# Performance work log

Measured on AMD Instinct MI355X. Metric: run time of the kernel, lower is better.

The kernel has to match this reference:

```python
import jax, jax.numpy as jnp
import numpy as np

D_MODEL = 512; D_STATE = 64; D_CONV = 4; HEADDIM = 64
D_INNER = 2 * D_MODEL              # expand=2
NHEADS = D_INNER // HEADDIM        # 16
CONV_DIM = D_INNER + 2 * D_STATE   # 1152
D_IN_PROJ = 2 * D_INNER + 2 * D_STATE + NHEADS  # 2192
BATCH, SEQ = 4, 1024
EPS = 1e-5


def rmsnorm(x, w):
    return x * jax.lax.rsqrt(jnp.mean(x * x, axis=-1, keepdims=True) + EPS) * w


def mamba2(u, in_w, conv_w, conv_b, dt_bias, A_log, D, gnorm_w, out_w):
    b, l, _ = u.shape
    zxbcdt = u @ in_w.T                                  # [b,l,D_IN_PROJ]
    z = zxbcdt[..., :D_INNER]
    xBC = zxbcdt[..., D_INNER:D_INNER + CONV_DIM]
    dt = jax.nn.softplus(zxbcdt[..., -NHEADS:] + dt_bias)  # [b,l,h]
    # causal depthwise conv1d (kernel D_CONV, left pad) + silu
    pad = jnp.pad(xBC, ((0, 0), (D_CONV - 1, 0), (0, 0)))
    acc = conv_b
    for k in range(D_CONV):
        acc = acc + pad[:, k:k + l, :] * conv_w[:, k]
    xBC = jax.nn.silu(acc)
    x = xBC[..., :D_INNER].reshape(b, l, NHEADS, HEADDIM)
    Bm = xBC[..., D_INNER:D_INNER + D_STATE]             # [b,l,n]
    Cm = xBC[..., D_INNER + D_STATE:]                    # [b,l,n]
    A = -jnp.exp(A_log)                                  # [h]
    decay = jnp.exp(dt * A)                              # [b,l,h]
    dtx = dt[..., None] * x                              # [b,l,h,p]

    def step(h, inp):
        dec, dx, Bt, Ct = inp
        h = h * dec[:, :, None, None] + dx[..., None] * Bt[:, None, None, :]
        y = jnp.einsum('bhpn,bn->bhp', h, Ct)
        return h, y

    h0 = jnp.zeros((b, NHEADS, HEADDIM, D_STATE), u.dtype)
    _, ys = jax.lax.scan(step, h0, (decay.transpose(1, 0, 2),
                                    dtx.transpose(1, 0, 2, 3),
                                    Bm.transpose(1, 0, 2),
                                    Cm.transpose(1, 0, 2)))
    y = ys.transpose(1, 0, 2, 3) + x * D[None, None, :, None]  # [b,l,h,p]
    y = y.reshape(b, l, D_INNER)
    y = rmsnorm(y * jax.nn.silu(z), gnorm_w)             # gated RMSNorm
    return y @ out_w.T


def setup_inputs() -> dict:
    key = jax.random.key(0)
    ks = iter(jax.random.split(key, 32))
    def rn(shape, scale=0.02):
        return jax.random.normal(next(ks), shape, dtype=jnp.float32) * scale
    inp = {
        'x': jax.random.normal(next(ks), (BATCH, SEQ, D_MODEL), dtype=jnp.float32),
        'norm_w': jnp.ones((D_MODEL,), jnp.float32),
    }
    for p in ('f', 'b'):
        inp[p + '_in_w'] = rn((D_IN_PROJ, D_MODEL))
        inp[p + '_conv_w'] = rn((CONV_DIM, D_CONV), 0.1)
        inp[p + '_conv_b'] = jnp.zeros((CONV_DIM,), jnp.float32)
        inp[p + '_dt_bias'] = rn((NHEADS,), 0.5)
        inp[p + '_A_log'] = jnp.log(jnp.arange(1, NHEADS + 1, dtype=jnp.float32))
        inp[p + '_D'] = jnp.ones((NHEADS,), jnp.float32)
        inp[p + '_gnorm_w'] = jnp.ones((D_INNER,), jnp.float32)
        inp[p + '_out_w'] = rn((D_MODEL, D_INNER))
    inp['proj_w'] = rn((D_MODEL, 2 * D_MODEL))
    return inp


def reference(x, norm_w,
              f_in_w, f_conv_w, f_conv_b, f_dt_bias, f_A_log, f_D, f_gnorm_w, f_out_w,
              b_in_w, b_conv_w, b_conv_b, b_dt_bias, b_A_log, b_D, b_gnorm_w, b_out_w,
              proj_w):
    h = rmsnorm(x, norm_w)
    fo = mamba2(h, f_in_w, f_conv_w, f_conv_b, f_dt_bias, f_A_log, f_D, f_gnorm_w, f_out_w)
    bo = jnp.flip(mamba2(jnp.flip(h, 1), b_in_w, b_conv_w, b_conv_b, b_dt_bias,
                         b_A_log, b_D, b_gnorm_w, b_out_w), 1)
    return x + jnp.concatenate([fo, bo], axis=-1) @ proj_w.T
```

## Files before the change

### kernel.cpp

```cpp
#include <hip/hip_runtime.h>
#include <math.h>

typedef unsigned short u16;
typedef __bf16  bf16x8 __attribute__((ext_vector_type(8)));
typedef float   f32x4  __attribute__((ext_vector_type(4)));
typedef unsigned short u16x8 __attribute__((ext_vector_type(8)));

#define SEQ 1024
#define MR  4096
#define DIP 2192
#define DI  1024
#define NH  16
#define CD  1152
#define NCH 32
#define CT  32
#define NIN (DIP*512)
#define NOUT (512*1024)
#define ZROW 4384

__device__ __forceinline__ u16 f2bf(float f) {
  union { float f; unsigned u; } v; v.f = f;
  unsigned r = v.u + 0x7FFFu + ((v.u >> 16) & 1u);
  return (u16)(r >> 16);
}
__device__ __forceinline__ float bf2f(u16 h) {
  union { unsigned u; float f; } v; v.u = ((unsigned)h) << 16; return v.f;
}
__device__ __forceinline__ void splitbf(float v, u16& h, u16& l) {
  h = f2bf(v); l = f2bf(v - bf2f(h));
}
__device__ __forceinline__ float sigm(float x){ return 1.f/(1.f+__expf(-x)); }

__device__ __forceinline__ unsigned packbf(float v) {
  u16 hh, ll; splitbf(v, hh, ll);
  return (unsigned)hh | ((unsigned)ll << 16);
}
__device__ __forceinline__ float unpackf(unsigned w) {
  return bf2f((u16)w) + bf2f((u16)(w >> 16));
}

__device__ __forceinline__ void unpack8(const unsigned* p, bf16x8& H, bf16x8& L) {
  uint4 a = *(const uint4*)p, b = *(const uint4*)(p+4);
  u16x8 hu, lu;
  hu[0]=(u16)a.x; lu[0]=(u16)(a.x>>16);
  hu[1]=(u16)a.y; lu[1]=(u16)(a.y>>16);
  hu[2]=(u16)a.z; lu[2]=(u16)(a.z>>16);
  hu[3]=(u16)a.w; lu[3]=(u16)(a.w>>16);
  hu[4]=(u16)b.x; lu[4]=(u16)(b.x>>16);
  hu[5]=(u16)b.y; lu[5]=(u16)(b.y>>16);
  hu[6]=(u16)b.z; lu[6]=(u16)(b.z>>16);
  hu[7]=(u16)b.w; lu[7]=(u16)(b.w>>16);
  H = __builtin_bit_cast(bf16x8, hu);
  L = __builtin_bit_cast(bf16x8, lu);
}
__device__ __forceinline__ void unpack8s(const unsigned* p, int stride, bf16x8& H, bf16x8& L) {
  u16x8 hu, lu;
  #pragma unroll
  for (int jj=0;jj<8;jj++){ unsigned w = p[(size_t)jj*stride]; hu[jj]=(u16)w; lu[jj]=(u16)(w>>16); }
  H = __builtin_bit_cast(bf16x8, hu);
  L = __builtin_bit_cast(bf16x8, lu);
}

__device__ __forceinline__ void gl16(const u16* g, u16* l) {
  __builtin_amdgcn_global_load_lds((const __attribute__((address_space(1))) void*)g,
                                   (__attribute__((address_space(3))) void*)l,
                                   16, 0, 0);
}

__global__ __launch_bounds__(256) void cast_all(
  const float* __restrict__ f_in, const float* __restrict__ b_in,
  const float* __restrict__ f_out, const float* __restrict__ b_out,
  const float* __restrict__ proj,
  u16* __restrict__ H, u16* __restrict__ L)
{
  int i = blockIdx.x*256 + threadIdx.x;
  constexpr int TOT = 2*NIN + 3*NOUT;
  if (i >= TOT) return;
  float v;
  if (i < NIN)               v = f_in[i];
  else if (i < 2*NIN)        v = b_in[i-NIN];
  else if (i < 2*NIN+NOUT)   v = f_out[i-2*NIN];
  else if (i < 2*NIN+2*NOUT) v = b_out[i-2*NIN-NOUT];
  else                       v = proj[i-2*NIN-2*NOUT];
  u16 hh, ll; splitbf(v, hh, ll);
  H[i] = hh; L[i] = ll;
}

__global__ __launch_bounds__(256) void rmsnorm_x(const float* __restrict__ x,
                                                 const float* __restrict__ w,
                                                 u16* __restrict__ hbh,
                                                 u16* __restrict__ hbl){
  int m = blockIdx.x, tid = threadIdx.x;
  const float* xr = x + (size_t)m*512;
  float2 v = *(const float2*)&xr[tid*2];
  float ss = v.x*v.x + v.y*v.y;
  #pragma unroll
  for (int off=32; off; off>>=1) ss += __shfl_xor(ss, off, 64);
  __shared__ float red[4];
  if ((tid&63)==0) red[tid>>6] = ss;
  __syncthreads();
  float total = red[0]+red[1]+red[2]+red[3];
  float rs = rsqrtf(total*(1.f/512.f) + 1e-5f);
  float2 w2 = *(const float2*)&w[tid*2];
  u16 h0,l0,h1,l1;
  splitbf(v.x*rs*w2.x, h0, l0);
  splitbf(v.y*rs*w2.y, h1, l1);
  *(unsigned*)&hbh[(size_t)m*512 + tid*2] = (unsigned)h0 | ((unsigned)h1<<16);
  *(unsigned*)&hbl[(size_t)m*512 + tid*2] = (unsigned)l0 | ((unsigned)l1<<16);
}

__global__ __launch_bounds__(256) void gemm_in(
    const u16* __restrict__ Ah, const u16* __restrict__ Al,
    const u16* __restrict__ Wh, const u16* __restrict__ Wl,
    float* __restrict__ C0)
{
  constexpr int K = 512;
  constexpr int N = DIP;
  __shared__ __align__(16) u16 sAh[128*32];
  __shared__ __align__(16) u16 sAl[128*32];
  __shared__ __align__(16) u16 sBh[128*32];
  __shared__ __align__(16) u16 sBl[128*32];
  const int tid = threadIdx.x;
  const int dir = blockIdx.z;
  const int m0 = blockIdx.x * 128;
  const int n0 = blockIdx.y * 128;
  const int lane = tid & 63;
  const int wid  = tid >> 6;
  const u16* wh_p = Wh + (size_t)dir*NIN;
  const u16* wl_p = Wl + (size_t)dir*NIN;
  const int j0 = wid, j1 = wid + 4;
  const int cp = lane & 3;
  auto goff = [&](int j, bool isB)->size_t {
    int row = 16*j + (lane>>2);
    int s = (row>>1) & 3;
    int kc = (cp ^ s) * 8;
    int grow;
    if (!isB) {
      grow = m0 + row;
      if (dir) grow = (grow & ~1023) + (1023 - (grow & 1023));
    } else {
      grow = n0 + row;
      if (grow >= N) grow = N-1;
    }
    return (size_t)grow*K + kc;
  };
  const size_t a0 = goff(j0,false), a1 = goff(j1,false);
  const size_t b0 = goff(j0,true),  b1 = goff(j1,true);
  const int wm = (wid & 1) * 64;
  const int wn = (wid >> 1) * 64;
  const int quad = lane >> 4;
  const int l16  = lane & 15;
  const int qx = quad ^ ((l16>>1)&3);
  const int baseA = ((wm + l16)*4 + qx)*8;
  const int baseB = ((wn + l16)*4 + qx)*8;
  f32x4 acc[4][4] = {};
  for (int kt = 0; kt < K; kt += 32) {
    __syncthreads();
    gl16(Ah + a0 + kt, &sAh[j0*512]);  gl16(Ah + a1 + kt, &sAh[j1*512]);
    gl16(Al + a0 + kt, &sAl[j0*512]);  gl16(Al + a1 + kt, &sAl[j1*512]);
    gl16(wh_p + b0 + kt, &sBh[j0*512]);  gl16(wh_p + b1 + kt, &sBh[j1*512]);
    gl16(wl_p + b0 + kt, &sBl[j0*512]);  gl16(wl_p + b1 + kt, &sBl[j1*512]);
    __syncthreads();
    bf16x8 ah[4], al[4], bh[4], bl[4];
    #pragma unroll
    for (int i=0;i<4;i++) {
      ah[i] = *(const bf16x8*)&sAh[baseA + i*512];
      al[i] = *(const bf16x8*)&sAl[baseA + i*512];
    }
    #pragma unroll
    for (int j=0;j<4;j++) {
      bh[j] = *(const bf16x8*)&sBh[baseB + j*512];
      bl[j] = *(const bf16x8*)&sBl[baseB + j*512];
    }
    #pragma unroll
    for (int i=0;i<4;i++)
      #pragma unroll
      for (int j=0;j<4;j++) {
        f32x4 t = __builtin_amdgcn_mfma_f32_16x16x32_bf16(ah[i], bl[j], acc[i][j], 0,0,0);
        t       = __builtin_amdgcn_mfma_f32_16x16x32_bf16(al[i], bh[j], t,         0,0,0);
        acc[i][j] = __builtin_amdgcn_mfma_f32_16x16x32_bf16(ah[i], bh[j], t,       0,0,0);
      }
  }
  #pragma unroll
  for (int i=0;i<4;i++)
  #pragma unroll
  for (int j=0;j<4;j++)
  #pragma unroll
  for (int r=0;r<4;r++) {
    int mo = m0 + wm + i*16 + quad*4 + r;
    int no = n0 + wn + j*16 + l16;
    if (no < N) C0[((size_t)dir*MR + mo)*DIP + no] = acc[i][j][r];
  }
}

template<int MODE>
__global__ __launch_bounds__(256) void gemm_out(
    const u16* __restrict__ Ah, const u16* __restrict__ Al,
    const u16* __restrict__ Wh, const u16* __restrict__ Wl,
    float* __restrict__ C0, const float* __restrict__ X0,
    u16* __restrict__ C1h, u16* __restrict__ C1l)
{
  constexpr int K = 1024;
  constexpr int AS = (MODE==1) ? ZROW : 1024;
  __shared__ __align__(16) u16 sAh[64*32];
  __shared__ __align__(16) u16 sAl[64*32];
  __shared__ __align__(16) u16 sBh[128*32];
  __shared__ __align__(16) u16 sBl[128*32];
  const int tid = threadIdx.x;
  const int dir = blockIdx.z;
  const int m0 = blockIdx.x * 64;
  const int n0 = blockIdx.y * 128;
  const int lane = tid & 63;
  const int wid  = tid >> 6;
  const u16* ah_p = Ah + ((MODE==1) ? (size_t)dir*MR*AS : 0);
  const u16* al_p = Al + ((MODE==1) ? (size_t)dir*MR*AS : 0);
  const u16* wh_p = Wh + ((MODE==1) ? (size_t)dir*NOUT : 0);
  const u16* wl_p = Wl + ((MODE==1) ? (size_t)dir*NOUT : 0);
  const int cp = lane & 3;
  auto goff = [&](int j, bool isB)->size_t {
    int row = 16*j + (lane>>2);
    int s = (row>>1) & 3;
    int kc = (cp ^ s) * 8;
    int grow = (isB ? n0 : m0) + row;
    return (size_t)grow*(isB ? (size_t)K : (size_t)AS) + kc;
  };
  const size_t a0 = goff(wid,false);
  const size_t b0 = goff(wid,true), b1 = goff(wid+4,true);
  const int quad = lane >> 4;
  const int l16  = lane & 15;
  const int qx = quad ^ ((l16>>1)&3);
  const int baseA = (l16*4 + qx)*8;
  const int baseB = ((wid*32 + l16)*4 + qx)*8;
  f32x4 acc[4][2] = {};
  for (int kt = 0; kt < K; kt += 32) {
    __syncthreads();
    gl16(ah_p + a0 + kt, &sAh[wid*512]);
    gl16(al_p + a0 + kt, &sAl[wid*512]);
    gl16(wh_p + b0 + kt, &sBh[wid*512]);  gl16(wh_p + b1 + kt, &sBh[(wid+4)*512]);
    gl16(wl_p + b0 + kt, &sBl[wid*512]);  gl16(wl_p + b1 + kt, &sBl[(wid+4)*512]);
    __syncthreads();
    bf16x8 ah[4], al[4], bh[2], bl[2];
    #pragma unroll
    for (int i=0;i<4;i++) {
      ah[i] = *(const bf16x8*)&sAh[baseA + i*512];
      al[i] = *(const bf16x8*)&sAl[baseA + i*512];
    }
    #pragma unroll
    for (int j=0;j<2;j++) {
      bh[j] = *(const bf16x8*)&sBh[baseB + j*512];
      bl[j] = *(const bf16x8*)&sBl[baseB + j*512];
    }
    #pragma unroll
    for (int i=0;i<4;i++)
      #pragma unroll
      for (int j=0;j<2;j++) {
        f32x4 t = __builtin_amdgcn_mfma_f32_16x16x32_bf16(ah[i], bl[j], acc[i][j], 0,0,0);
        t       = __builtin_amdgcn_mfma_f32_16x16x32_bf16(al[i], bh[j], t,         0,0,0);
        acc[i][j] = __builtin_amdgcn_mfma_f32_16x16x32_bf16(ah[i], bh[j], t,       0,0,0);
      }
  }
  #pragma unroll
  for (int i=0;i<4;i++)
  #pragma unroll
  for (int j=0;j<2;j++)
  #pragma unroll
  for (int r=0;r<4;r++) {
    int mo = m0 + i*16 + quad*4 + r;
    int no = n0 + wid*32 + j*16 + l16;
    float v = acc[i][j][r];
    if (MODE==1) {
      int ro = mo;
      if (dir) ro = (mo & ~1023) + (1023 - (mo & 1023));
      u16 hh, ll; splitbf(v, hh, ll);
      C1h[(size_t)ro*DI + dir*512 + no] = hh;
      C1l[(size_t)ro*DI + dir*512 + no] = ll;
    } else {
      C0[(size_t)mo*512 + no] = v + X0[(size_t)mo*512 + no];
    }
  }
}

__global__ __launch_bounds__(320) void conv_dt(
  const float* __restrict__ Z,
  const float* __restrict__ f_cw, const float* __restrict__ f_cb,
  const float* __restrict__ b_cw, const float* __restrict__ b_cb,
  const float* __restrict__ f_dtb, const float* __restrict__ b_dtb,
  unsigned* __restrict__ xconv,
  unsigned* __restrict__ Bc, unsigned* __restrict__ Cc,
  float* __restrict__ dtq)
{
  int bm = blockIdx.x;
  int dir = bm >> 12;
  int t = bm & 1023;
  const float* cw  = dir ? b_cw : f_cw;
  const float* cb  = dir ? b_cb : f_cb;
  const float* dtb = dir ? b_dtb : f_dtb;
  int tid = threadIdx.x;
  if (tid < 288) {
    int c0 = tid*4;
    const float* zbase = Z + (size_t)(bm-3)*DIP + 1024 + c0;
    float4 w0 = *(const float4*)&cw[c0*4];
    float4 w1 = *(const float4*)&cw[(c0+1)*4];
    float4 w2 = *(const float4*)&cw[(c0+2)*4];
    float4 w3 = *(const float4*)&cw[(c0+3)*4];
    float4 z0 = {0,0,0,0}, z1 = {0,0,0,0}, z2 = {0,0,0,0};
    float4 z3 = *(const float4*)(zbase + 3*(size_t)DIP);
    if (t >= 3) {
      z0 = *(const float4*)(zbase);
      z1 = *(const float4*)(zbase + (size_t)DIP);
      z2 = *(const float4*)(zbase + 2*(size_t)DIP);
    } else {
      if (t >= 1) z2 = *(const float4*)(zbase + 2*(size_t)DIP);
      if (t >= 2) z1 = *(const float4*)(zbase + (size_t)DIP);
    }
    float4 a = *(const float4*)&cb[c0];
    a.x += z0.x*w0.x + z1.x*w0.y + z2.x*w0.z + z3.x*w0.w;
    a.y += z0.y*w1.x + z1.y*w1.y + z2.y*w1.z + z3.y*w1.w;
    a.z += z0.z*w2.x + z1.z*w2.y + z2.z*w2.z + z3.z*w2.w;
    a.w += z0.w*w3.x + z1.w*w3.y + z2.w*w3.z + z3.w*w3.w;
    float4 v;
    v.x = a.x * sigm(a.x); v.y = a.y * sigm(a.y);
    v.z = a.z * sigm(a.z); v.w = a.w * sigm(a.w);
    uint4 pv;
    pv.x = packbf(v.x); pv.y = packbf(v.y);
    pv.z = packbf(v.z); pv.w = packbf(v.w);
    if (c0 < 1024)      *(uint4*)&xconv[(size_t)bm*DI + c0] = pv;
    else if (c0 < 1088) *(uint4*)&Bc[(size_t)bm*64 + (c0-1024)] = pv;
    else                *(uint4*)&Cc[(size_t)bm*64 + (c0-1088)] = pv;
  }
  if (tid < NH) {
    float dtraw = Z[(size_t)bm*DIP + 2176 + tid] + dtb[tid];
    float dt = (dtraw > 20.f) ? dtraw : log1pf(__expf(dtraw));
    dtq[(size_t)bm*NH + tid] = dt;
  }
}

__global__ __launch_bounds__(256) void scan_mfma(
  const float* __restrict__ dtq, const unsigned* __restrict__ xconv,
  const unsigned* __restrict__ Bc, const unsigned* __restrict__ Cc,
  const float* __restrict__ f_Al, const float* __restrict__ b_Al,
  float* __restrict__ yraw, float* __restrict__ cumdec, float* __restrict__ S)
{
  __shared__ __align__(16) u16 sMh[4][32*40];
  __shared__ __align__(16) u16 sMl[4][32*40];
  __shared__ float scum[4][32];
  __shared__ float sdt[4][32];
  int bx = blockIdx.x;
  int hq = bx & 3, chunk = (bx>>2)&(NCH-1), dirb = bx>>7;
  int w = threadIdx.x >> 6, lane = threadIdx.x & 63;
  int h = hq*4 + w;
  int base_row = dirb*1024 + chunk*CT;
  const int quad = lane >> 4, l16 = lane & 15;
  const float* Al = (dirb >= 4) ? b_Al : f_Al;
  float A = -__expf(Al[h]);
  float dtl = 0.f, cum = 0.f;
  if (lane < 32) { dtl = dtq[(size_t)(base_row + lane)*16 + h]; cum = dtl; }
  #pragma unroll
  for (int off=1; off<32; off<<=1) {
    int src = (lane >= off) ? lane-off : lane;
    float o = __shfl(cum, src);
    if (lane >= off && lane < 32) cum += o;
  }
  if (lane < 32) {
    sdt[w][lane]  = dtl;
    scum[w][lane] = cum;
    cumdec[(size_t)(base_row + lane)*16 + h] = __expf(A*cum);
  }
  bf16x8 chf[2][2], clf[2][2], bhf[2][2], blf[2][2];
  #pragma unroll
  for (int i=0;i<2;i++)
  #pragma unroll
  for (int kk=0;kk<2;kk++) {
    unpack8(Cc + (size_t)(base_row + 16*i + l16)*64 + kk*32 + quad*8, chf[i][kk], clf[i][kk]);
    unpack8(Bc + (size_t)(base_row + 16*i + l16)*64 + kk*32 + quad*8, bhf[i][kk], blf[i][kk]);
  }
  f32x4 g[2][2];
  __builtin_amdgcn_s_setprio(1);
  #pragma unroll
  for (int i=0;i<2;i++)
  #pragma unroll
  for (int j=0;j<2;j++) {
    f32x4 acc = {};
    #pragma unroll
    for (int kk=0;kk<2;kk++) {
      acc = __builtin_amdgcn_mfma_f32_16x16x32_bf16(chf[i][kk], blf[j][kk], acc, 0,0,0);
      acc = __builtin_amdgcn_mfma_f32_16x16x32_bf16(clf[i][kk], bhf[j][kk], acc, 0,0,0);
      acc = __builtin_amdgcn_mfma_f32_16x16x32_bf16(chf[i][kk], bhf[j][kk], acc, 0,0,0);
    }
    g[i][j] = acc;
  }
  __builtin_amdgcn_s_setprio(0);
  float ctt[2][4];
  #pragma unroll
  for (int i=0;i<2;i++)
  #pragma unroll
  for (int r=0;r<4;r++) ctt[i][r] = scum[w][16*i + quad*4 + r];
  #pragma unroll
  for (int j=0;j<2;j++) {
    int s = 16*j + l16;
    float cts = scum[w][s];
    float dts = sdt[w][s];
    #pragma unroll
    for (int i=0;i<2;i++)
    #pragma unroll
    for (int r=0;r<4;r++) {
      int t = 16*i + quad*4 + r;
      float mv = (s <= t) ? g[i][j][r] * __expf(A*(ctt[i][r]-cts)) * dts : 0.f;
      u16 hh, ll; splitbf(mv, hh, ll);
      sMh[w][t*40 + s] = hh;
      sMl[w][t*40 + s] = ll;
    }
  }
  bf16x8 xhf[4], xlf[4];
  const unsigned* xp = xconv + (size_t)(base_row + quad*8)*1024 + h*64 + l16;
  #pragma unroll
  for (int jp=0;jp<4;jp++) unpack8s(xp + 16*jp, 1024, xhf[jp], xlf[jp]);
  bf16x8 mhf[2], mlf[2];
  #pragma unroll
  for (int i=0;i<2;i++) {
    mhf[i] = *(const bf16x8*)&sMh[w][(16*i + l16)*40 + quad*8];
    mlf[i] = *(const bf16x8*)&sMl[w][(16*i + l16)*40 + quad*8];
  }
  __builtin_amdgcn_s_setprio(1);
  #pragma unroll
  for (int i=0;i<2;i++)
  #pragma unroll
  for (int jp=0;jp<4;jp++) {
    f32x4 acc = {};
    acc = __builtin_amdgcn_mfma_f32_16x16x32_bf16(mhf[i], xlf[jp], acc, 0,0,0);
    acc = __builtin_amdgcn_mfma_f32_16x16x32_bf16(mlf[i], xhf[jp], acc, 0,0,0);
    acc = __builtin_amdgcn_mfma_f32_16x16x32_bf16(mhf[i], xhf[jp], acc, 0,0,0);
    #pragma unroll
    for (int r=0;r<4;r++)
      yraw[(size_t)(base_row + 16*i + quad*4 + r)*1024 + h*64 + 16*jp + l16] = acc[r];
  }
  __builtin_amdgcn_s_setprio(0);
  float wv[8];
  float ct31 = scum[w][31];
  #pragma unroll
  for (int jj=0;jj<8;jj++) {
    int s = quad*8 + jj;
    wv[jj] = sdt[w][s] * __expf(A*(ct31 - scum[w][s]));
  }
  bf16x8 wbh[4], wbl[4];
  #pragma unroll
  for (int j2=0;j2<4;j2++) {
    u16x8 hu, lu; u16 hh, ll;
    #pragma unroll
    for (int jj=0;jj<8;jj++) {
      float b = unpackf(Bc[(size_t)(base_row + quad*8 + jj)*64 + 16*j2 + l16]);
      splitbf(wv[jj]*b, hh, ll); hu[jj]=hh; lu[jj]=ll;
    }
    wbh[j2] = __builtin_bit_cast(bf16x8, hu);
    wbl[j2] = __builtin_bit_cast(bf16x8, lu);
  }
  size_t inst = ((size_t)(dirb*16+h)*NCH + chunk)*4096;
  __builtin_amdgcn_s_setprio(1);
  #pragma unroll
  for (int mp=0;mp<4;mp++)
  #pragma unroll
  for (int j2=0;j2<4;j2++) {
    f32x4 acc = {};
    acc = __builtin_amdgcn_mfma_f32_16x16x32_bf16(xhf[mp], wbl[j2], acc, 0,0,0);
    acc = __builtin_amdgcn_mfma_f32_16x16x32_bf16(xlf[mp], wbh[j2], acc, 0,0,0);
    acc = __builtin_amdgcn_mfma_f32_16x16x32_bf16(xhf[mp], wbh[j2], acc, 0,0,0);
    #pragma unroll
    for (int r=0;r<4;r++)
      S[inst + (size_t)(16*mp + quad*4 + r)*64 + 16*j2 + l16] = acc[r];
  }
  __builtin_amdgcn_s_setprio(0);
}

__global__ __launch_bounds__(256) void scan_comb(
  const float* __restrict__ cumdec, float* __restrict__ S)
{
  int ih = blockIdx.x >> 4;
  int sub = blockIdx.x & 15;
  int dirb = ih >> 4, h = ih & 15;
  int elem = sub*256 + threadIdx.x;
  size_t base = (size_t)ih*NCH*4096 + elem;
  float hr = 0.f;
  for (int c=0;c<NCH;c++) {
    float P = cumdec[((size_t)(dirb*1024 + c*CT + CT-1))*16 + h];
    float s = S[base + c*4096];
    S[base + c*4096] = __builtin_bit_cast(float, packbf(hr));
    hr = fmaf(hr, P, s);
  }
}

__global__ __launch_bounds__(1024) void scan_y2_gate(
  const unsigned* __restrict__ Cc, const float* __restrict__ cumdec,
  const float* __restrict__ S, const float* __restrict__ yraw,
  const unsigned* __restrict__ xconv, const float* Z, u16* zt,
  const float* __restrict__ f_D, const float* __restrict__ b_D,
  const float* __restrict__ f_gw, const float* __restrict__ b_gw)
{
  __shared__ float vbuf[32][1028];
  __shared__ float red[32][17];
  __shared__ float rsb[32];
  int bx = blockIdx.x;
  int chunk = bx & (NCH-1), dirb = bx >> 5;
  int w = threadIdx.x >> 6, lane = threadIdx.x & 63;
  int h = w;
  int dir = dirb >> 2;
  int row0 = dirb*1024 + chunk*CT;
  const int quad = lane>>4, l16 = lane&15;
  const float* Dp  = dir ? b_D  : f_D;
  const float* gwp = dir ? b_gw : f_gw;
  float Dv = Dp[h];

  f32x4 acc[2][4] = {};
  float at[2][4] = {};
  if (chunk > 0) {
    size_t inst = ((size_t)(dirb*16+h)*NCH + chunk)*4096;
    #pragma unroll
    for (int i=0;i<2;i++)
    #pragma unroll
    for (int r=0;r<4;r++)
      at[i][r] = cumdec[(size_t)(row0 + 16*i + quad*4 + r)*16 + h];
    bf16x8 chf[2][2], clf[2][2];
    #pragma unroll
    for (int i=0;i<2;i++)
    #pragma unroll
    for (int kk=0;kk<2;kk++)
      unpack8(Cc + (size_t)(row0 + 16*i + l16)*64 + kk*32 + quad*8, chf[i][kk], clf[i][kk]);
    const unsigned* Sp = (const unsigned*)S;
    __builtin_amdgcn_s_setprio(1);
    #pragma unroll
    for (int j=0;j<4;j++) {
      bf16x8 hhf[2], hlf[2];
      #pragma unroll
      for (int kk=0;kk<2;kk++)
        unpack8(Sp + inst + (size_t)(16*j + l16)*64 + kk*32 + quad*8, hhf[kk], hlf[kk]);
      #pragma unroll
      for (int i=0;i<2;i++) {
        f32x4 a2 = acc[i][j];
        #pragma unroll
        for (int kk=0;kk<2;kk++) {
          a2 = __builtin_amdgcn_mfma_f32_16x16x32_bf16(chf[i][kk], hlf[kk], a2, 0,0,0);
          a2 = __builtin_amdgcn_mfma_f32_16x16x32_bf16(clf[i][kk], hhf[kk], a2, 0,0,0);
          a2 = __builtin_amdgcn_mfma_f32_16x16x32_bf16(chf[i][kk], hhf[kk], a2, 0,0,0);
        }
        acc[i][j] = a2;
      }
    }
    __builtin_amdgcn_s_setprio(0);
  }
  float pss[2][4] = {};
  #pragma unroll
  for (int i=0;i<2;i++)
  #pragma unroll
  for (int r=0;r<4;r++) {
    int t = 16*i + quad*4 + r;
    size_t g = (size_t)(row0 + t);
    #pragma unroll
    for (int j=0;j<4;j++) {
      int c = h*64 + 16*j + l16;
      float yv = yraw[g*1024 + c];
      float xv = unpackf(xconv[g*1024 + c]);
      float zv = Z[g*DIP + c];
      float v = (yv + xv*Dv + at[i][r]*acc[i][j][r]) * (zv * sigm(zv));
      vbuf[t][c] = v;
      pss[i][r] += v*v;
    }
  }
  #pragma unroll
  for (int i=0;i<2;i++)
  #pragma unroll
  for (int r=0;r<4;r++) {
    float s2 = pss[i][r];
    s2 += __shfl_xor(s2, 1, 64);
    s2 += __shfl_xor(s2, 2, 64);
    s2 += __shfl_xor(s2, 4, 64);
    s2 += __shfl_xor(s2, 8, 64);
    if (l16 == 0) red[16*i + quad*4 + r][w] = s2;
  }
  __syncthreads();
  if (threadIdx.x < 32) {
    int t = threadIdx.x;
    float tot = 0.f;
    #pragma unroll
    for (int ww=0; ww<16; ww++) tot += red[t][ww];
    rsb[t] = rsqrtf(tot*(1.f/1024.f) + 1e-5f);
  }
  __syncthreads();
  #pragma unroll
  for (int i=0;i<2;i++)
  #pragma unroll
  for (int r=0;r<4;r++) {
    int t = 16*i + quad*4 + r;
    size_t g = (size_t)(row0 + t);
    float rs = rsb[t];
    #pragma unroll
    for (int j=0;j<4;j++) {
      int c = h*64 + 16*j + l16;
      float o = vbuf[t][c] * rs * gwp[c];
      u16 hh, ll; splitbf(o, hh, ll);
      zt[g*ZROW + 2048 + c] = hh;
      zt[g*ZROW + 3072 + c] = ll;
    }
  }
}

extern "C" void kernel_launch(void* const* d_in, const int* in_sizes, int n_in,
                              void* d_out, int out_size, void* d_ws, size_t ws_size,
                              hipStream_t stream)
{
  const float* x        = (const float*)d_in[0];
  const float* norm_w   = (const float*)d_in[1];
  const float* f_in_w   = (const float*)d_in[2];
  const float* f_conv_w = (const float*)d_in[3];
  const float* f_conv_b = (const float*)d_in[4];
  const float* f_dt_bias= (const float*)d_in[5];
  const float* f_A_log  = (const float*)d_in[6];
  const float* f_D      = (const float*)d_in[7];
  const float* f_gw     = (const float*)d_in[8];
  const float* f_out_w  = (const float*)d_in[9];
  const float* b_in_w   = (const float*)d_in[10];
  const float* b_conv_w = (const float*)d_in[11];
  const float* b_conv_b = (const float*)d_in[12];
  const float* b_dt_bias= (const float*)d_in[13];
  const float* b_A_log  = (const float*)d_in[14];
  const float* b_D      = (const float*)d_in[15];
  const float* b_gw     = (const float*)d_in[16];
  const float* b_out_w  = (const float*)d_in[17];
  const float* proj_w   = (const float*)d_in[18];

  char* ws = (char*)d_ws;
  size_t off = 0;
  auto alloc = [&](size_t bytes)->char* {
    char* p = ws + off; off = (off + bytes + 255) & ~(size_t)255; return p;
  };
  constexpr size_t WTOT = 2*(size_t)NIN + 3*(size_t)NOUT;
  u16*   hbh   = (u16*)  alloc((size_t)MR*512*2);
  u16*   hbl   = (u16*)  alloc((size_t)MR*512*2);
  u16*   wH    = (u16*)  alloc(WTOT*2);
  u16*   wL    = (u16*)  alloc(WTOT*2);
  float* Z     = (float*)alloc(2*(size_t)MR*DIP*4);
  unsigned* xconv = (unsigned*)alloc(2*(size_t)MR*DI*4);
  unsigned* Bc    = (unsigned*)alloc(2*(size_t)MR*64*4);
  unsigned* Cc    = (unsigned*)alloc(2*(size_t)MR*64*4);
  float* dtq   = (float*)alloc(2*(size_t)MR*NH*4);
  float* cumdec= (float*)alloc(2*(size_t)MR*NH*4);
  float* S     = (float*)alloc((size_t)4096*4096*4);
  float* yraw  = (float*)alloc(2*(size_t)MR*DI*4);
  u16* wih = wH;                   u16* wil = wL;
  u16* woh = wH + 2*(size_t)NIN;   u16* wol = wL + 2*(size_t)NIN;
  u16* wph = woh + 2*(size_t)NOUT; u16* wpl = wol + 2*(size_t)NOUT;
  u16* ycath = (u16*)((char*)S);
  u16* ycatl = (u16*)((char*)S + ((size_t)MR*DI*2));

  cast_all<<<(int)((WTOT+255)/256),256,0,stream>>>(f_in_w, b_in_w, f_out_w, b_out_w, proj_w, wH, wL);

  rmsnorm_x<<<MR,256,0,stream>>>(x, norm_w, hbh, hbl);
  gemm_in<<<dim3(32,18,2),256,0,stream>>>(hbh, hbl, wih, wil, Z);
  conv_dt<<<2*MR,320,0,stream>>>(Z, f_conv_w, f_conv_b, b_conv_w, b_conv_b,
                                 f_dt_bias, b_dt_bias, xconv, Bc, Cc, dtq);
  scan_mfma<<<1024,256,0,stream>>>(dtq, xconv, Bc, Cc, f_A_log, b_A_log,
                                   yraw, cumdec, S);
  scan_comb<<<2048,256,0,stream>>>(cumdec, S);
  scan_y2_gate<<<256,1024,0,stream>>>(Cc, cumdec, S, yraw, xconv, Z, (u16*)Z,
                                      f_D, b_D, f_gw, b_gw);
  gemm_out<1><<<dim3(64,4,2),256,0,stream>>>((u16*)Z + 2048, (u16*)Z + 3072,
                                             woh, wol, nullptr, nullptr, ycath, ycatl);
  gemm_out<2><<<dim3(64,4,1),256,0,stream>>>(ycath, ycatl, wph, wpl,
                                             (float*)d_out, x, nullptr, nullptr);
}
```

Measured before the change: 368.1 us.

## Fold out-projection into final projection by precombining weights

Precomputes the combined weight proj_w[:, dir-half] @ out_w for each direction in a small weight-only GEMM, then replaces the two chained output GEMMs with one fused GEMM. That GEMM reads the gated activations from both directions, with the backward direction's rows reversed, and adds the residual. This removes the intermediate ycat round trip and one full M×1024×512 GEMM pass. The cost is a small extra weight-combine kernel, re-rounding of the combined weights to a bf16 hi/lo split, and an 8-wave block layout with separate loader waves.

After: 380.4 us. 3.3% more time.

```diff
diff --git a/kernel.cpp b/kernel.cpp
--- a/kernel.cpp
+++ b/kernel.cpp
@@ -71,7 +71,7 @@
   const float* __restrict__ f_in, const float* __restrict__ b_in,
   const float* __restrict__ f_out, const float* __restrict__ b_out,
   const float* __restrict__ proj,
-  u16* __restrict__ H, u16* __restrict__ L)
+  u16* __restrict__ H, u16* __restrict__ L, unsigned* __restrict__ wpk)
 {
   int i = blockIdx.x*256 + threadIdx.x;
   constexpr int TOT = 2*NIN + 3*NOUT;
@@ -82,8 +82,55 @@
   else if (i < 2*NIN+NOUT)   v = f_out[i-2*NIN];
   else if (i < 2*NIN+2*NOUT) v = b_out[i-2*NIN-NOUT];
   else                       v = proj[i-2*NIN-2*NOUT];
-  u16 hh, ll; splitbf(v, hh, ll);
-  H[i] = hh; L[i] = ll;
+  if (i < 2*NIN) {
+    u16 hh, ll; splitbf(v, hh, ll);
+    H[i] = hh; L[i] = ll;
+  } else {
+    wpk[i - 2*NIN] = packbf(v);
+  }
+}
+
+__global__ __launch_bounds__(256) void wcomb(
+  const unsigned* __restrict__ wpk,
+  u16* __restrict__ Wch, u16* __restrict__ Wcl)
+{
+  int d = blockIdx.z;
+  int o0 = blockIdx.x*64, p0 = blockIdx.y*128;
+  int wv = threadIdx.x>>6, lane = threadIdx.x&63;
+  int quad = lane>>4, l16 = lane&15;
+  const unsigned* owp = wpk + (size_t)d*NOUT;
+  const unsigned* pjp = wpk + 2*(size_t)NOUT;
+  int pc = p0 + wv*32;
+  f32x4 acc[4][2] = {};
+  for (int kt=0; kt<512; kt+=32) {
+    bf16x8 ahf[4], alf[4], bhf[2], blf[2];
+    #pragma unroll
+    for (int ia=0; ia<4; ia++)
+      unpack8(pjp + (size_t)(o0 + 16*ia + l16)*1024 + d*512 + kt + quad*8, ahf[ia], alf[ia]);
+    #pragma unroll
+    for (int jb=0; jb<2; jb++)
+      unpack8s(owp + (size_t)(kt + quad*8)*1024 + pc + 16*jb + l16, 1024, bhf[jb], blf[jb]);
+    #pragma unroll
+    for (int ia=0; ia<4; ia++)
+      #pragma unroll
+      for (int jb=0; jb<2; jb++) {
+        f32x4 t = __builtin_amdgcn_mfma_f32_16x16x32_bf16(ahf[ia], blf[jb], acc[ia][jb], 0,0,0);
+        t       = __builtin_amdgcn_mfma_f32_16x16x32_bf16(alf[ia], bhf[jb], t,           0,0,0);
+        acc[ia][jb] = __builtin_amdgcn_mfma_f32_16x16x32_bf16(ahf[ia], bhf[jb], t,       0,0,0);
+      }
+  }
+  #pragma unroll
+  for (int ia=0; ia<4; ia++)
+  #pragma unroll
+  for (int jb=0; jb<2; jb++)
+  #pragma unroll
+  for (int r=0; r<4; r++) {
+    int o = o0 + 16*ia + quad*4 + r;
+    int p = pc + 16*jb + l16;
+    u16 hh, ll; splitbf(acc[ia][jb][r], hh, ll);
+    Wch[(size_t)d*NOUT + (size_t)o*1024 + p] = hh;
+    Wcl[(size_t)d*NOUT + (size_t)o*1024 + p] = ll;
+  }
 }
 
 __global__ __launch_bounds__(256) void rmsnorm_x(const float* __restrict__ x,
@@ -193,90 +240,85 @@
   }
 }
 
-template<int MODE>
-__global__ __launch_bounds__(256) void gemm_out(
-    const u16* __restrict__ Ah, const u16* __restrict__ Al,
-    const u16* __restrict__ Wh, const u16* __restrict__ Wl,
-    float* __restrict__ C0, const float* __restrict__ X0,
-    u16* __restrict__ C1h, u16* __restrict__ C1l)
-{
-  constexpr int K = 1024;
-  constexpr int AS = (MODE==1) ? ZROW : 1024;
+__global__ __launch_bounds__(512) void gemm_final(
+    const u16* __restrict__ zt, const u16* __restrict__ Wch, const u16* __restrict__ Wcl,
+    const float* __restrict__ X0, float* __restrict__ out)
+{
   __shared__ __align__(16) u16 sAh[64*32];
   __shared__ __align__(16) u16 sAl[64*32];
   __shared__ __align__(16) u16 sBh[128*32];
   __shared__ __align__(16) u16 sBl[128*32];
   const int tid = threadIdx.x;
-  const int dir = blockIdx.z;
-  const int m0 = blockIdx.x * 64;
-  const int n0 = blockIdx.y * 128;
-  const int lane = tid & 63;
-  const int wid  = tid >> 6;
-  const u16* ah_p = Ah + ((MODE==1) ? (size_t)dir*MR*AS : 0);
-  const u16* al_p = Al + ((MODE==1) ? (size_t)dir*MR*AS : 0);
-  const u16* wh_p = Wh + ((MODE==1) ? (size_t)dir*NOUT : 0);
-  const u16* wl_p = Wl + ((MODE==1) ? (size_t)dir*NOUT : 0);
+  const int lane = tid & 63, wid = tid >> 6;
+  const int m0 = blockIdx.x * 64, n0 = blockIdx.y * 128;
   const int cp = lane & 3;
-  auto goff = [&](int j, bool isB)->size_t {
-    int row = 16*j + (lane>>2);
-    int s = (row>>1) & 3;
-    int kc = (cp ^ s) * 8;
-    int grow = (isB ? n0 : m0) + row;
-    return (size_t)grow*(isB ? (size_t)K : (size_t)AS) + kc;
-  };
-  const size_t a0 = goff(wid,false);
-  const size_t b0 = goff(wid,true), b1 = goff(wid+4,true);
-  const int quad = lane >> 4;
-  const int l16  = lane & 15;
+  const int quad = lane >> 4, l16 = lane & 15;
+  const int wm = (wid & 1) * 32;
+  const int wn = (wid >> 1) * 32;
   const int qx = quad ^ ((l16>>1)&3);
-  const int baseA = (l16*4 + qx)*8;
-  const int baseB = ((wid*32 + l16)*4 + qx)*8;
-  f32x4 acc[4][2] = {};
-  for (int kt = 0; kt < K; kt += 32) {
-    __syncthreads();
-    gl16(ah_p + a0 + kt, &sAh[wid*512]);
-    gl16(al_p + a0 + kt, &sAl[wid*512]);
-    gl16(wh_p + b0 + kt, &sBh[wid*512]);  gl16(wh_p + b1 + kt, &sBh[(wid+4)*512]);
-    gl16(wl_p + b0 + kt, &sBl[wid*512]);  gl16(wl_p + b1 + kt, &sBl[(wid+4)*512]);
-    __syncthreads();
-    bf16x8 ah[4], al[4], bh[2], bl[2];
-    #pragma unroll
-    for (int i=0;i<4;i++) {
-      ah[i] = *(const bf16x8*)&sAh[baseA + i*512];
-      al[i] = *(const bf16x8*)&sAl[baseA + i*512];
-    }
-    #pragma unroll
-    for (int j=0;j<2;j++) {
-      bh[j] = *(const bf16x8*)&sBh[baseB + j*512];
-      bl[j] = *(const bf16x8*)&sBl[baseB + j*512];
-    }
-    #pragma unroll
-    for (int i=0;i<4;i++)
+  const int baseA = ((wm + l16)*4 + qx)*8;
+  const int baseB = ((wn + l16)*4 + qx)*8;
+  f32x4 acc[2][2] = {};
+  const int jb0 = (wid-4)*2, jb1 = jb0+1;
+  for (int dir=0; dir<2; ++dir) {
+    size_t aoff=0, boff0=0, boff1=0;
+    if (wid < 4) {
+      int row = 16*wid + (lane>>2);
+      int s = (row>>1) & 3;
+      int kc = (cp ^ s) * 8;
+      int grow = m0 + row;
+      if (dir) grow = (grow & ~1023) + (1023 - (grow & 1023));
+      aoff = (size_t)(dir*MR + grow)*ZROW + kc;
+    } else {
+      int row0 = 16*jb0 + (lane>>2);
+      int s0 = (row0>>1) & 3;
+      boff0 = (size_t)dir*NOUT + (size_t)(n0 + row0)*1024 + (cp ^ s0)*8;
+      int row1 = 16*jb1 + (lane>>2);
+      int s1 = (row1>>1) & 3;
+      boff1 = (size_t)dir*NOUT + (size_t)(n0 + row1)*1024 + (cp ^ s1)*8;
+    }
+    for (int kt = 0; kt < 1024; kt += 32) {
+      __syncthreads();
+      if (wid < 4) {
+        gl16(zt + 2048 + aoff + kt, &sAh[wid*512]);
+        gl16(zt + 3072 + aoff + kt, &sAl[wid*512]);
+      } else {
+        gl16(Wch + boff0 + kt, &sBh[jb0*512]);
+        gl16(Wch + boff1 + kt, &sBh[jb1*512]);
+        gl16(Wcl + boff0 + kt, &sBl[jb0*512]);
+        gl16(Wcl + boff1 + kt, &sBl[jb1*512]);
+      }
+      __syncthreads();
+      bf16x8 ah[2], al[2], bh[2], bl[2];
+      #pragma unroll
+      for (int i=0;i<2;i++) {
+        ah[i] = *(const bf16x8*)&sAh[baseA + i*512];
+        al[i] = *(const bf16x8*)&sAl[baseA + i*512];
+      }
       #pragma unroll
       for (int j=0;j<2;j++) {
-        f32x4 t = __builtin_amdgcn_mfma_f32_16x16x32_bf16(ah[i], bl[j], acc[i][j], 0,0,0);
-        t       = __builtin_amdgcn_mfma_f32_16x16x32_bf16(al[i], bh[j], t,         0,0,0);
-        acc[i][j] = __builtin_amdgcn_mfma_f32_16x16x32_bf16(ah[i], bh[j], t,       0,0,0);
+        bh[j] = *(const bf16x8*)&sBh[baseB + j*512];
+        bl[j] = *(const bf16x8*)&sBl[baseB + j*512];
       }
-  }
-  #pragma unroll
-  for (int i=0;i<4;i++)
+      #pragma unroll
+      for (int i=0;i<2;i++)
+        #pragma unroll
+        for (int j=0;j<2;j++) {
+          f32x4 t = __builtin_amdgcn_mfma_f32_16x16x32_bf16(ah[i], bl[j], acc[i][j], 0,0,0);
+          t       = __builtin_amdgcn_mfma_f32_16x16x32_bf16(al[i], bh[j], t,         0,0,0);
+          acc[i][j] = __builtin_amdgcn_mfma_f32_16x16x32_bf16(ah[i], bh[j], t,       0,0,0);
+        }
+    }
+  }
+  #pragma unroll
+  for (int i=0;i<2;i++)
   #pragma unroll
   for (int j=0;j<2;j++)
   #pragma unroll
   for (int r=0;r<4;r++) {
-    int mo = m0 + i*16 + quad*4 + r;
-    int no = n0 + wid*32 + j*16 + l16;
-    float v = acc[i][j][r];
-    if (MODE==1) {
-      int ro = mo;
-      if (dir) ro = (mo & ~1023) + (1023 - (mo & 1023));
-      u16 hh, ll; splitbf(v, hh, ll);
-      C1h[(size_t)ro*DI + dir*512 + no] = hh;
-      C1l[(size_t)ro*DI + dir*512 + no] = ll;
-    } else {
-      C0[(size_t)mo*512 + no] = v + X0[(size_t)mo*512 + no];
-    }
+    int mo = m0 + wm + 16*i + quad*4 + r;
+    int no = n0 + wn + 16*j + l16;
+    out[(size_t)mo*512 + no] = acc[i][j][r] + X0[(size_t)mo*512 + no];
   }
 }
 
@@ -631,11 +673,13 @@
   auto alloc = [&](size_t bytes)->char* {
     char* p = ws + off; off = (off + bytes + 255) & ~(size_t)255; return p;
   };
-  constexpr size_t WTOT = 2*(size_t)NIN + 3*(size_t)NOUT;
   u16*   hbh   = (u16*)  alloc((size_t)MR*512*2);
   u16*   hbl   = (u16*)  alloc((size_t)MR*512*2);
-  u16*   wH    = (u16*)  alloc(WTOT*2);
-  u16*   wL    = (u16*)  alloc(WTOT*2);
+  u16*   wH    = (u16*)  alloc(2*(size_t)NIN*2);
+  u16*   wL    = (u16*)  alloc(2*(size_t)NIN*2);
+  unsigned* wpk = (unsigned*)alloc(3*(size_t)NOUT*4);
+  u16*   Wch   = (u16*)  alloc(2*(size_t)NOUT*2);
+  u16*   Wcl   = (u16*)  alloc(2*(size_t)NOUT*2);
   float* Z     = (float*)alloc(2*(size_t)MR*DIP*4);
   unsigned* xconv = (unsigned*)alloc(2*(size_t)MR*DI*4);
   unsigned* Bc    = (unsigned*)alloc(2*(size_t)MR*64*4);
@@ -644,13 +688,12 @@
   float* cumdec= (float*)alloc(2*(size_t)MR*NH*4);
   float* S     = (float*)alloc((size_t)4096*4096*4);
   float* yraw  = (float*)alloc(2*(size_t)MR*DI*4);
-  u16* wih = wH;                   u16* wil = wL;
-  u16* woh = wH + 2*(size_t)NIN;   u16* wol = wL + 2*(size_t)NIN;
-  u16* wph = woh + 2*(size_t)NOUT; u16* wpl = wol + 2*(size_t)NOUT;
-  u16* ycath = (u16*)((char*)S);
-  u16* ycatl = (u16*)((char*)S + ((size_t)MR*DI*2));
-
-  cast_all<<<(int)((WTOT+255)/256),256,0,stream>>>(f_in_w, b_in_w, f_out_w, b_out_w, proj_w, wH, wL);
+  u16* wih = wH;  u16* wil = wL;
+
+  constexpr int TOT = 2*NIN + 3*NOUT;
+  cast_all<<<(TOT+255)/256,256,0,stream>>>(f_in_w, b_in_w, f_out_w, b_out_w, proj_w,
+                                           wH, wL, wpk);
+  wcomb<<<dim3(8,8,2),256,0,stream>>>(wpk, Wch, Wcl);
 
   rmsnorm_x<<<MR,256,0,stream>>>(x, norm_w, hbh, hbl);
   gemm_in<<<dim3(32,18,2),256,0,stream>>>(hbh, hbl, wih, wil, Z);
@@ -661,8 +704,5 @@
   scan_comb<<<2048,256,0,stream>>>(cumdec, S);
   scan_y2_gate<<<256,1024,0,stream>>>(Cc, cumdec, S, yraw, xconv, Z, (u16*)Z,
                                       f_D, b_D, f_gw, b_gw);
-  gemm_out<1><<<dim3(64,4,2),256,0,stream>>>((u16*)Z + 2048, (u16*)Z + 3072,
-                                             woh, wol, nullptr, nullptr, ycath, ycatl);
-  gemm_out<2><<<dim3(64,4,1),256,0,stream>>>(ycath, ycatl, wph, wpl,
-                                             (float*)d_out, x, nullptr, nullptr);
-}
+  gemm_final<<<dim3(64,4),512,0,stream>>>((u16*)Z, Wch, Wcl, x, (float*)d_out);
+}
```
